# Kernel tuning notes

Hardware: AMD Instinct MI355X
Metric: run time of the kernel (lower is better)

The kernel has to match this reference:

```python
import jax, jax.numpy as jnp
import numpy as np

N_NODES = 100000
N_EDGES = 2000000
F_IN = 32
HID = 32
N_CLASS = 40


def _gru_cell(m, h, wih, whh, bih, bhh):
    # torch.nn.GRUCell math; wih/whh: [3H, H_in], gates ordered r, z, n
    gi = m @ wih.T + bih
    gh = h @ whh.T + bhh
    i_r, i_z, i_n = jnp.split(gi, 3, axis=-1)
    h_r, h_z, h_n = jnp.split(gh, 3, axis=-1)
    r = jax.nn.sigmoid(i_r + h_r)
    z = jax.nn.sigmoid(i_z + h_z)
    n = jnp.tanh(i_n + r * h_n)
    return (1.0 - z) * n + z * h


def _gated_conv(x, edge_index, edge_weight, w_proj, w_msg, wih, whh, bih, bhh):
    h = x @ w_proj                                   # [N, out]
    msg = (h @ w_msg)[edge_index[0]] * edge_weight[:, None]  # gather src -> [E, out]
    agg = jax.ops.segment_sum(msg, edge_index[1], num_segments=N_NODES)  # scatter-add to dst
    return _gru_cell(agg, h, wih, whh, bih, bhh)


def setup_inputs() -> dict:
    key = jax.random.key(0)
    ks = jax.random.split(key, 16)
    s = 0.1
    return {
        "x": jax.random.normal(ks[0], (N_NODES, F_IN), jnp.float32),
        "edge_index": jax.random.randint(ks[1], (2, N_EDGES), 0, N_NODES, jnp.int64),
        "edge_weight": jax.random.uniform(ks[2], (N_EDGES,), jnp.float32),
        "W1_proj": jax.random.normal(ks[3], (F_IN, HID), jnp.float32) * s,
        "W1_msg": jax.random.normal(ks[4], (HID, HID), jnp.float32) * s,
        "gru1_wih": jax.random.normal(ks[5], (3 * HID, HID), jnp.float32) * s,
        "gru1_whh": jax.random.normal(ks[6], (3 * HID, HID), jnp.float32) * s,
        "gru1_bih": jax.random.normal(ks[7], (3 * HID,), jnp.float32) * s,
        "gru1_bhh": jax.random.normal(ks[8], (3 * HID,), jnp.float32) * s,
        "W2_proj": jax.random.normal(ks[9], (HID, N_CLASS), jnp.float32) * s,
        "W2_msg": jax.random.normal(ks[10], (N_CLASS, N_CLASS), jnp.float32) * s,
        "gru2_wih": jax.random.normal(ks[11], (3 * N_CLASS, N_CLASS), jnp.float32) * s,
        "gru2_whh": jax.random.normal(ks[12], (3 * N_CLASS, N_CLASS), jnp.float32) * s,
        "gru2_bih": jax.random.normal(ks[13], (3 * N_CLASS,), jnp.float32) * s,
        "gru2_bhh": jax.random.normal(ks[14], (3 * N_CLASS,), jnp.float32) * s,
    }


def reference(x, edge_index, edge_weight, W1_proj, W1_msg, gru1_wih, gru1_whh,
              gru1_bih, gru1_bhh, W2_proj, W2_msg, gru2_wih, gru2_whh,
              gru2_bih, gru2_bhh):
    # eval mode: dropout is identity
    h = _gated_conv(x, edge_index, edge_weight, W1_proj, W1_msg,
                    gru1_wih, gru1_whh, gru1_bih, gru1_bhh)
    h = jax.nn.relu(h)
    h = _gated_conv(h, edge_index, edge_weight, W2_proj, W2_msg,
                    gru2_wih, gru2_whh, gru2_bih, gru2_bhh)
    return jax.nn.log_softmax(h, axis=-1)
```

## Files before the change

### kernel.cpp

```cpp
#include <hip/hip_runtime.h>
#include <math.h>

#define NN 100000
#define NP 100032
#define NE 2000000
#define FIN 32
#define H 32
#define NC 40

#define NBK 196
#define BSH 9
#define CAP 11264
#define EPT 16
#define EPB (256 * EPT)

typedef _Float16 half_t;
typedef __attribute__((ext_vector_type(8))) _Float16 half8;
typedef __attribute__((ext_vector_type(4))) _Float16 half4;
typedef __attribute__((ext_vector_type(4))) float f32x4;

__device__ __forceinline__ float sigm_(float x) {
    return 1.0f / (1.0f + __expf(-x));
}
__device__ __forceinline__ float tanh_(float x) {
    x = fminf(fmaxf(x, -20.0f), 20.0f);
    float e = __expf(2.0f * x);
    return (e - 1.0f) / (e + 1.0f);
}

__global__ __launch_bounds__(256) void kA_bucket(const int* __restrict__ ei,
                                                 const float* __restrict__ ew,
                                                 int* __restrict__ gcur,
                                                 long long* __restrict__ rec) {
    __shared__ long long recs[EPB];
    __shared__ int gdst[EPB];
    __shared__ int cnt[NBK], base[NBK], sofs[NBK];
    __shared__ int ssc[256];
    int tid = threadIdx.x;
    for (int i = tid; i < NBK; i += 256) cnt[i] = 0;
    __syncthreads();
    int e0 = blockIdx.x * EPB;
    int dcache[EPT];
#pragma unroll
    for (int i = 0; i < EPT; ++i) {
        int e = e0 + i * 256 + tid;
        dcache[i] = (e < NE) ? ei[NE + e] : -1;
        if (e < NE) atomicAdd(&cnt[dcache[i] >> BSH], 1);
    }
    __syncthreads();
    int cv = (tid < NBK) ? cnt[tid] : 0;
    ssc[tid] = cv;
    __syncthreads();
    for (int off = 1; off < 256; off <<= 1) {
        int v = (tid >= off) ? ssc[tid - off] : 0;
        __syncthreads();
        ssc[tid] += v;
        __syncthreads();
    }
    if (tid < NBK) {
        sofs[tid] = ssc[tid] - cv;
        base[tid] = atomicAdd(&gcur[tid], cv);
        cnt[tid] = 0;
    }
    __syncthreads();
#pragma unroll
    for (int i = 0; i < EPT; ++i) {
        int e = e0 + i * 256 + tid;
        if (e < NE) {
            int d = dcache[i], s = ei[e];
            int b = d >> BSH;
            int r = atomicAdd(&cnt[b], 1);
            int slot = sofs[b] + r;
            int pos = base[b] + r;
            int lo = s | ((d & 511) << 17);
            recs[slot] = (long long)(unsigned)lo |
                         ((long long)__float_as_int(ew[e]) << 32);
            gdst[slot] = (pos < CAP) ? (b * CAP + pos) : -1;
        }
    }
    __syncthreads();
    int nrec = min(EPB, NE - e0);
    for (int i = tid; i < nrec; i += 256) {
        int gd = gdst[i];
        if (gd >= 0) rec[gd] = recs[i];
    }
}

__global__ __launch_bounds__(256) void kB_sort(const int* __restrict__ gcur,
                                               const int2* __restrict__ rec,
                                               int2* __restrict__ evs,
                                               int* __restrict__ ofs,
                                               int* __restrict__ ocn) {
    __shared__ int hist[512], lofs[512], ssc[256];
    int tid = threadIdx.x, b = blockIdx.x;
    int nb0 = b << BSH;
    int nnodes = min(512, NN - nb0);
    int cntb = min(gcur[b], CAP);
    hist[tid] = 0;
    hist[tid + 256] = 0;
    __syncthreads();
    const int2* rb = rec + (size_t)b * CAP;
    for (int i = tid; i < cntb; i += 256)
        atomicAdd(&hist[(rb[i].x >> 17) & 511], 1);
    __syncthreads();
    int ps = hist[2 * tid] + hist[2 * tid + 1];
    ssc[tid] = ps;
    __syncthreads();
    for (int off = 1; off < 256; off <<= 1) {
        int v = (tid >= off) ? ssc[tid - off] : 0;
        __syncthreads();
        ssc[tid] += v;
        __syncthreads();
    }
    int ex = ssc[tid] - ps;
    lofs[2 * tid] = ex;
    lofs[2 * tid + 1] = ex + hist[2 * tid];
    __syncthreads();
    for (int l = tid; l < nnodes; l += 256) {
        ofs[nb0 + l] = b * CAP + lofs[l];
        ocn[nb0 + l] = hist[l];
    }
    hist[tid] = 0;
    hist[tid + 256] = 0;
    __syncthreads();
    int2* eb = evs + (size_t)b * CAP;
    for (int i = tid; i < cntb; i += 256) {
        int2 r = rb[i];
        int dl = (r.x >> 17) & 511;
        int rk = atomicAdd(&hist[dl], 1);
        eb[lofs[dl] + rk] = make_int2(r.x & 0x1FFFF, r.y);
    }
}

__global__ __launch_bounds__(256) void k_wpre(const float* __restrict__ W2m,
                                              const float* __restrict__ wih2,
                                              float* __restrict__ M2,
                                              int* __restrict__ gcur) {
    int i = blockIdx.x * 256 + threadIdx.x;
    if (i < NBK) gcur[i] = 0;
    if (i >= NC * 3 * NC) return;
    int u = i / (3 * NC), col = i % (3 * NC);
    float acc = 0.f;
#pragma unroll
    for (int t = 0; t < NC; ++t) acc += W2m[u * NC + t] * wih2[col * NC + t];
    M2[i] = acc;
}

__global__ __launch_bounds__(256) void k_wc(const float* __restrict__ W1m,
                                            const float* __restrict__ wih1,
                                            const float* __restrict__ W2p,
                                            const float* __restrict__ M2,
                                            const float* __restrict__ whh1,
                                            const float* __restrict__ whh2,
                                            half_t* __restrict__ W1sw,
                                            half_t* __restrict__ W2sw) {
    int i = blockIdx.x * 256 + threadIdx.x;
    if (i < 8192) {
        int j = i & 7, lane = (i >> 3) & 63, ct = (i >> 9) & 7, s = i >> 12;
        int k = s * 32 + (lane >> 4) * 8 + j;
        int col = ct * 16 + (lane & 15);
        int g = col >> 5, jj = col & 31;
        float v = 0.f;
        if (g <= 2) {
            if (k < 32) {
                float acc = 0.f;
#pragma unroll
                for (int t = 0; t < H; ++t) acc += W1m[k * H + t] * wih1[(g * H + jj) * H + t];
                v = acc;
            } else if (g < 2) {
                v = whh1[(g * H + jj) * H + (k - 32)];
            }
        } else {
            if (k >= 32) v = whh1[(2 * H + jj) * H + (k - 32)];
        }
        W1sw[i] = (half_t)v;
    } else if (i < 8192 + 18432) {
        int i2 = i - 8192;
        int j = i2 & 7, lane = (i2 >> 3) & 63;
        int tt = i2 >> 9;
        int ct = tt % 12, s = tt / 12;
        int k = s * 32 + (lane >> 4) * 8 + j;
        int col = ct * 16 + (lane & 15);
        int g = col / 48, jj = col % 48;
        float v = 0.f;
        if (jj < NC) {
            if (g <= 2) {
                if (k < 32) {
                    float acc = 0.f;
#pragma unroll
                    for (int u = 0; u < NC; ++u)
                        acc += W2p[k * NC + u] * M2[u * 3 * NC + g * NC + jj];
                    v = acc;
                } else if (k < 72 && g < 2) {
                    v = whh2[(g * NC + jj) * NC + (k - 32)];
                }
            } else {
                if (k >= 32 && k < 72) v = whh2[(2 * NC + jj) * NC + (k - 32)];
            }
        }
        W2sw[i2] = (half_t)v;
    }
}

__global__ __launch_bounds__(256) void k1_proj(const float* __restrict__ x,
                                               const float* __restrict__ Wp,
                                               half_t* __restrict__ Xc1) {
    __shared__ float sWp[FIN * H];
    __shared__ float sx[8][FIN];
    int tid = threadIdx.x;
    for (int i = tid; i < FIN * H; i += 256) sWp[i] = Wp[i];
    int nb = blockIdx.x * 8;
    int nl = tid >> 5, j = tid & 31;
    int n = nb + nl;
    if (n < NN) sx[nl][j] = x[(size_t)n * FIN + j];
    __syncthreads();
    float acc = 0.f;
#pragma unroll
    for (int k = 0; k < FIN; ++k) acc += sx[nl][k] * sWp[k * H + j];
    if (n < NN) Xc1[(size_t)n * 64 + 32 + j] = (half_t)acc;
}

__global__ __launch_bounds__(320) void k4_proj2(const half_t* __restrict__ Hh,
                                                const float* __restrict__ Wp,
                                                half_t* __restrict__ Xc2) {
    __shared__ float sWp[FIN * NC];
    __shared__ float shn[8][FIN];
    int tid = threadIdx.x;
    for (int i = tid; i < FIN * NC; i += 320) sWp[i] = Wp[i];
    int nb = blockIdx.x * 8;
    if (tid < 256) {
        int r = tid >> 5, c = tid & 31;
        shn[r][c] = (float)Hh[(size_t)(nb + r) * 32 + c];
    }
    if (tid < 192) {
        int r = tid / 24, c = tid % 24;
        Xc2[(size_t)(nb + r) * 96 + 72 + c] = (half_t)0.f;
    }
    __syncthreads();
    int nl = tid / NC, j = tid % NC;
    int n = nb + nl;
    float acc = 0.f;
#pragma unroll
    for (int k = 0; k < FIN; ++k) acc += shn[nl][k] * sWp[k * NC + j];
    if (n < NN) Xc2[(size_t)n * 96 + 32 + j] = (half_t)acc;
}

template <int SSTR4, int DSTR>
__global__ __launch_bounds__(256) void k_aggh(const int* __restrict__ ofs,
                                              const int* __restrict__ ocn,
                                              const int2* __restrict__ evs,
                                              const half_t* __restrict__ src,
                                              half_t* __restrict__ dst) {
    int idx = blockIdx.x * 256 + threadIdx.x;
    int n = idx >> 3, q = idx & 7;
    if (n >= NN) return;
    const half4* s4 = (const half4*)src + q;
    const long long* ev8 = (const long long*)evs;
    int s0 = ofs[n], c = ocn[n];
    int e1 = s0 + c;
    float acc[4] = {0.f, 0.f, 0.f, 0.f};
    int e = s0;
    for (; e + 4 <= e1; e += 4) {
        long long r0 = __builtin_nontemporal_load(ev8 + e);
        long long r1 = __builtin_nontemporal_load(ev8 + e + 1);
        long long r2 = __builtin_nontemporal_load(ev8 + e + 2);
        long long r3 = __builtin_nontemporal_load(ev8 + e + 3);
        half4 h0 = s4[(size_t)(r0 & 0x1FFFF) * SSTR4];
        half4 h1 = s4[(size_t)(r1 & 0x1FFFF) * SSTR4];
        half4 h2 = s4[(size_t)(r2 & 0x1FFFF) * SSTR4];
        half4 h3 = s4[(size_t)(r3 & 0x1FFFF) * SSTR4];
        float w0 = __int_as_float((int)(r0 >> 32));
        float w1 = __int_as_float((int)(r1 >> 32));
        float w2 = __int_as_float((int)(r2 >> 32));
        float w3 = __int_as_float((int)(r3 >> 32));
#pragma unroll
        for (int t = 0; t < 4; ++t) {
            acc[t] += w0 * (float)h0[t];
            acc[t] += w1 * (float)h1[t];
            acc[t] += w2 * (float)h2[t];
            acc[t] += w3 * (float)h3[t];
        }
    }
    for (; e < e1; ++e) {
        long long r = __builtin_nontemporal_load(ev8 + e);
        float w = __int_as_float((int)(r >> 32));
        half4 hv = s4[(size_t)(r & 0x1FFFF) * SSTR4];
#pragma unroll
        for (int t = 0; t < 4; ++t) acc[t] += w * (float)hv[t];
    }
    half4 o;
#pragma unroll
    for (int t = 0; t < 4; ++t) o[t] = (half_t)acc[t];
    *(half4*)(dst + (size_t)n * DSTR + q * 4) = o;
}

__global__ __launch_bounds__(256) void k3m(const half_t* __restrict__ Xc1,
                                           const half8* __restrict__ W1sw,
                                           const float* __restrict__ bih,
                                           const float* __restrict__ bhh,
                                           half_t* __restrict__ Hh) {
    int tid = threadIdx.x;
    int wave = tid >> 6, lane = tid & 63;
    int m16 = lane & 15, q = lane >> 4;
    int nb = blockIdx.x * 64 + wave * 16;
    const half8* xr = (const half8*)(Xc1 + (size_t)(nb + m16) * 64);
    half8 a0 = xr[q];
    half8 a1 = xr[4 + q];
    f32x4 acc[8];
#pragma unroll
    for (int ct = 0; ct < 8; ++ct) acc[ct] = (f32x4){0.f, 0.f, 0.f, 0.f};
#pragma unroll
    for (int ct = 0; ct < 8; ++ct) {
        acc[ct] = __builtin_amdgcn_mfma_f32_16x16x32_f16(a0, W1sw[ct * 64 + lane], acc[ct], 0, 0, 0);
        acc[ct] = __builtin_amdgcn_mfma_f32_16x16x32_f16(a1, W1sw[(8 + ct) * 64 + lane], acc[ct], 0, 0, 0);
    }
#pragma unroll
    for (int ct = 0; ct < 2; ++ct) {
        int j = ct * 16 + m16;
        float br = bih[j] + bhh[j];
        float bz = bih[H + j] + bhh[H + j];
        float bi = bih[2 * H + j], bh = bhh[2 * H + j];
#pragma unroll
        for (int m = 0; m < 4; ++m) {
            int node = nb + q * 4 + m;
            float r = sigm_(acc[ct][m] + br);
            float z = sigm_(acc[2 + ct][m] + bz);
            float ng = tanh_(acc[4 + ct][m] + bi + r * (acc[6 + ct][m] + bh));
            float hj = (float)Xc1[(size_t)node * 64 + 32 + j];
            float o = fmaxf((1.f - z) * ng + z * hj, 0.f);
            if (node < NN) Hh[(size_t)node * 32 + j] = (half_t)o;
        }
    }
}

__global__ __launch_bounds__(256) void k6m(const half_t* __restrict__ Xc2,
                                           const half8* __restrict__ W2sw,
                                           const float* __restrict__ bih,
                                           const float* __restrict__ bhh,
                                           float* __restrict__ out) {
    int tid = threadIdx.x;
    int wave = tid >> 6, lane = tid & 63;
    int m16 = lane & 15, q = lane >> 4;
    int nb = blockIdx.x * 64 + wave * 16;
    const half8* xr = (const half8*)(Xc2 + (size_t)(nb + m16) * 96);
    half8 a0 = xr[q], a1 = xr[4 + q], a2 = xr[8 + q];
    f32x4 acc[12];
#pragma unroll
    for (int ct = 0; ct < 12; ++ct) acc[ct] = (f32x4){0.f, 0.f, 0.f, 0.f};
#pragma unroll
    for (int ct = 0; ct < 12; ++ct) {
        acc[ct] = __builtin_amdgcn_mfma_f32_16x16x32_f16(a0, W2sw[ct * 64 + lane], acc[ct], 0, 0, 0);
        acc[ct] = __builtin_amdgcn_mfma_f32_16x16x32_f16(a1, W2sw[(12 + ct) * 64 + lane], acc[ct], 0, 0, 0);
        acc[ct] = __builtin_amdgcn_mfma_f32_16x16x32_f16(a2, W2sw[(24 + ct) * 64 + lane], acc[ct], 0, 0, 0);
    }
    float v[3][4];
#pragma unroll
    for (int ct = 0; ct < 3; ++ct) {
        int j = ct * 16 + m16;
        int jc = (j < NC) ? j : (NC - 1);
        float br = bih[jc] + bhh[jc];
        float bz = bih[NC + jc] + bhh[NC + jc];
        float bi = bih[2 * NC + jc], bh = bhh[2 * NC + jc];
#pragma unroll
        for (int m = 0; m < 4; ++m) {
            int node = nb + q * 4 + m;
            float r = sigm_(acc[ct][m] + br);
            float z = sigm_(acc[3 + ct][m] + bz);
            float ng = tanh_(acc[6 + ct][m] + bi + r * (acc[9 + ct][m] + bh));
            float hj = (float)Xc2[(size_t)node * 96 + 32 + jc];
            v[ct][m] = (1.f - z) * ng + z * hj;
        }
    }
    bool v2ok = (m16 < 8);
#pragma unroll
    for (int m = 0; m < 4; ++m) {
        float mx = fmaxf(v[0][m], v[1][m]);
        if (v2ok) mx = fmaxf(mx, v[2][m]);
#pragma unroll
        for (int d = 1; d < 16; d <<= 1) mx = fmaxf(mx, __shfl_xor(mx, d));
        float se = __expf(v[0][m] - mx) + __expf(v[1][m] - mx) +
                   (v2ok ? __expf(v[2][m] - mx) : 0.f);
#pragma unroll
        for (int d = 1; d < 16; d <<= 1) se += __shfl_xor(se, d);
        float ls = mx + __logf(se);
        int node = nb + q * 4 + m;
        if (node < NN) {
            out[(size_t)node * NC + m16] = v[0][m] - ls;
            out[(size_t)node * NC + 16 + m16] = v[1][m] - ls;
            if (v2ok) out[(size_t)node * NC + 32 + m16] = v[2][m] - ls;
        }
    }
}

extern "C" void kernel_launch(void* const* d_in, const int* in_sizes, int n_in,
                              void* d_out, int out_size, void* d_ws, size_t ws_size,
                              hipStream_t stream) {
    const float* x = (const float*)d_in[0];
    const int* ei = (const int*)d_in[1];
    const float* ew = (const float*)d_in[2];
    const float* W1p = (const float*)d_in[3];
    const float* W1m = (const float*)d_in[4];
    const float* g1wih = (const float*)d_in[5];
    const float* g1whh = (const float*)d_in[6];
    const float* g1bih = (const float*)d_in[7];
    const float* g1bhh = (const float*)d_in[8];
    const float* W2p = (const float*)d_in[9];
    const float* W2m = (const float*)d_in[10];
    const float* g2wih = (const float*)d_in[11];
    const float* g2whh = (const float*)d_in[12];
    const float* g2bih = (const float*)d_in[13];
    const float* g2bhh = (const float*)d_in[14];
    float* ws = (float*)d_ws;

    half_t* Xc = (half_t*)ws;
    half_t* Hh = (half_t*)(ws + 4801536);
    int2* rec = (int2*)ws;
    int2* evs = (int2*)(ws + 6402048);
    int* ofs = (int*)(ws + 10817536);
    int* ocn = (int*)(ws + 10917536);
    int* gcur = (int*)(ws + 11017536);
    half_t* W1sw = (half_t*)(ws + 11017792);
    half_t* W2sw = W1sw + 8192;
    float* M2 = ws + 11031104;
    float* out = (float*)d_out;

    k_wpre<<<(NC * 3 * NC + 255) / 256, 256, 0, stream>>>(W2m, g2wih, M2, gcur);
    kA_bucket<<<(NE + EPB - 1) / EPB, 256, 0, stream>>>(ei, ew, gcur, (long long*)rec);
    kB_sort<<<NBK, 256, 0, stream>>>(gcur, rec, evs, ofs, ocn);
    k_wc<<<(8192 + 18432 + 255) / 256, 256, 0, stream>>>(
        W1m, g1wih, W2p, M2, g1whh, g2whh, W1sw, W2sw);

    k1_proj<<<NN / 8, 256, 0, stream>>>(x, W1p, Xc);
    k_aggh<16, 64><<<(NN * 8 + 255) / 256, 256, 0, stream>>>(ofs, ocn, evs, Xc + 32, Xc);
    k3m<<<NP / 64, 256, 0, stream>>>(Xc, (const half8*)W1sw, g1bih, g1bhh, Hh);

    k4_proj2<<<NN / 8, 320, 0, stream>>>(Hh, W2p, Xc);
    k_aggh<8, 96><<<(NN * 8 + 255) / 256, 256, 0, stream>>>(ofs, ocn, evs, Hh, Xc);
    k6m<<<NP / 64, 256, 0, stream>>>(Xc, (const half8*)W2sw, g2bih, g2bhh, out);
}
```

Before: 313.2 us.

## Split per-node edge lists into source-range slices with block-synchronized gather

The bucket sort now bins edges by destination and by one of four source-index ranges. Each node's offsets and counts are stored per slice, with the four counts packed as 8-bit fields. The aggregation kernel walks the slices in order and calls __syncthreads between them, so all threads of a block gather from the same region of the source feature array together, aiming for better L2 locality. Layer 1 also writes a compact 32-wide copy of the projected features so the gather reads rows half as wide. The costs are more offset arrays, extra block barriers, and a silent limit of 255 edges per node per slice; bucket capacity is also lowered.

```diff
diff --git a/kernel.cpp b/kernel.cpp
--- a/kernel.cpp
+++ b/kernel.cpp
@@ -10,7 +10,8 @@
 
 #define NBK 196
 #define BSH 9
-#define CAP 11264
+#define CAP 10880
+#define NSL 4
 #define EPT 16
 #define EPB (256 * EPT)
 
@@ -89,22 +90,29 @@
 __global__ __launch_bounds__(256) void kB_sort(const int* __restrict__ gcur,
                                                const int2* __restrict__ rec,
                                                int2* __restrict__ evs,
-                                               int* __restrict__ ofs,
-                                               int* __restrict__ ocn) {
-    __shared__ int hist[512], lofs[512], ssc[256];
+                                               int* __restrict__ ofs2,
+                                               int* __restrict__ cnt4) {
+    __shared__ int hist[2048], lofs[2048], ssc[256];
     int tid = threadIdx.x, b = blockIdx.x;
     int nb0 = b << BSH;
     int nnodes = min(512, NN - nb0);
     int cntb = min(gcur[b], CAP);
-    hist[tid] = 0;
-    hist[tid + 256] = 0;
+    for (int i = tid; i < 2048; i += 256) hist[i] = 0;
     __syncthreads();
     const int2* rb = rec + (size_t)b * CAP;
-    for (int i = tid; i < cntb; i += 256)
-        atomicAdd(&hist[(rb[i].x >> 17) & 511], 1);
-    __syncthreads();
-    int ps = hist[2 * tid] + hist[2 * tid + 1];
-    ssc[tid] = ps;
+    for (int i = tid; i < cntb; i += 256) {
+        int rx = rb[i].x;
+        int bin = (((rx & 0x1FFFF) >> 15) << BSH) | ((rx >> 17) & 511);
+        atomicAdd(&hist[bin], 1);
+    }
+    __syncthreads();
+    int base = tid * 8, ls = 0, lh[8];
+#pragma unroll
+    for (int j = 0; j < 8; ++j) {
+        lh[j] = hist[base + j];
+        ls += lh[j];
+    }
+    ssc[tid] = ls;
     __syncthreads();
     for (int off = 1; off < 256; off <<= 1) {
         int v = (tid >= off) ? ssc[tid - off] : 0;
@@ -112,23 +120,30 @@
         ssc[tid] += v;
         __syncthreads();
     }
-    int ex = ssc[tid] - ps;
-    lofs[2 * tid] = ex;
-    lofs[2 * tid + 1] = ex + hist[2 * tid];
+    int ex = ssc[tid] - ls;
+#pragma unroll
+    for (int j = 0; j < 8; ++j) {
+        lofs[base + j] = ex;
+        ex += lh[j];
+    }
     __syncthreads();
     for (int l = tid; l < nnodes; l += 256) {
-        ofs[nb0 + l] = b * CAP + lofs[l];
-        ocn[nb0 + l] = hist[l];
-    }
-    hist[tid] = 0;
-    hist[tid + 256] = 0;
+        int c0 = hist[l], c1 = hist[512 + l], c2 = hist[1024 + l], c3 = hist[1536 + l];
+        cnt4[nb0 + l] = c0 | (c1 << 8) | (c2 << 16) | (c3 << 24);
+        ofs2[0 * NN + nb0 + l] = b * CAP + lofs[l];
+        ofs2[1 * NN + nb0 + l] = b * CAP + lofs[512 + l];
+        ofs2[2 * NN + nb0 + l] = b * CAP + lofs[1024 + l];
+        ofs2[3 * NN + nb0 + l] = b * CAP + lofs[1536 + l];
+    }
+    __syncthreads();
+    for (int i = tid; i < 2048; i += 256) hist[i] = 0;
     __syncthreads();
     int2* eb = evs + (size_t)b * CAP;
     for (int i = tid; i < cntb; i += 256) {
         int2 r = rb[i];
-        int dl = (r.x >> 17) & 511;
-        int rk = atomicAdd(&hist[dl], 1);
-        eb[lofs[dl] + rk] = make_int2(r.x & 0x1FFFF, r.y);
+        int bin = (((r.x & 0x1FFFF) >> 15) << BSH) | ((r.x >> 17) & 511);
+        int rk = atomicAdd(&hist[bin], 1);
+        eb[lofs[bin] + rk] = make_int2(r.x & 0x1FFFF, r.y);
     }
 }
 
@@ -204,7 +219,8 @@
 
 __global__ __launch_bounds__(256) void k1_proj(const float* __restrict__ x,
                                                const float* __restrict__ Wp,
-                                               half_t* __restrict__ Xc1) {
+                                               half_t* __restrict__ Xc1,
+                                               half_t* __restrict__ Hd) {
     __shared__ float sWp[FIN * H];
     __shared__ float sx[8][FIN];
     int tid = threadIdx.x;
@@ -217,7 +233,11 @@
     float acc = 0.f;
 #pragma unroll
     for (int k = 0; k < FIN; ++k) acc += sx[nl][k] * sWp[k * H + j];
-    if (n < NN) Xc1[(size_t)n * 64 + 32 + j] = (half_t)acc;
+    if (n < NN) {
+        half_t hv = (half_t)acc;
+        Xc1[(size_t)n * 64 + 32 + j] = hv;
+        Hd[(size_t)n * 32 + j] = hv;
+    }
 }
 
 __global__ __launch_bounds__(320) void k4_proj2(const half_t* __restrict__ Hh,
@@ -245,48 +265,51 @@
     if (n < NN) Xc2[(size_t)n * 96 + 32 + j] = (half_t)acc;
 }
 
-template <int SSTR4, int DSTR>
-__global__ __launch_bounds__(256) void k_aggh(const int* __restrict__ ofs,
-                                              const int* __restrict__ ocn,
+template <int DSTR>
+__global__ __launch_bounds__(256) void k_aggh(const int* __restrict__ ofs2,
+                                              const int* __restrict__ cnt4,
                                               const int2* __restrict__ evs,
                                               const half_t* __restrict__ src,
                                               half_t* __restrict__ dst) {
     int idx = blockIdx.x * 256 + threadIdx.x;
     int n = idx >> 3, q = idx & 7;
-    if (n >= NN) return;
     const half4* s4 = (const half4*)src + q;
     const long long* ev8 = (const long long*)evs;
-    int s0 = ofs[n], c = ocn[n];
-    int e1 = s0 + c;
+    int cw = cnt4[n];
     float acc[4] = {0.f, 0.f, 0.f, 0.f};
-    int e = s0;
-    for (; e + 4 <= e1; e += 4) {
-        long long r0 = __builtin_nontemporal_load(ev8 + e);
-        long long r1 = __builtin_nontemporal_load(ev8 + e + 1);
-        long long r2 = __builtin_nontemporal_load(ev8 + e + 2);
-        long long r3 = __builtin_nontemporal_load(ev8 + e + 3);
-        half4 h0 = s4[(size_t)(r0 & 0x1FFFF) * SSTR4];
-        half4 h1 = s4[(size_t)(r1 & 0x1FFFF) * SSTR4];
-        half4 h2 = s4[(size_t)(r2 & 0x1FFFF) * SSTR4];
-        half4 h3 = s4[(size_t)(r3 & 0x1FFFF) * SSTR4];
-        float w0 = __int_as_float((int)(r0 >> 32));
-        float w1 = __int_as_float((int)(r1 >> 32));
-        float w2 = __int_as_float((int)(r2 >> 32));
-        float w3 = __int_as_float((int)(r3 >> 32));
-#pragma unroll
-        for (int t = 0; t < 4; ++t) {
-            acc[t] += w0 * (float)h0[t];
-            acc[t] += w1 * (float)h1[t];
-            acc[t] += w2 * (float)h2[t];
-            acc[t] += w3 * (float)h3[t];
-        }
-    }
-    for (; e < e1; ++e) {
-        long long r = __builtin_nontemporal_load(ev8 + e);
-        float w = __int_as_float((int)(r >> 32));
-        half4 hv = s4[(size_t)(r & 0x1FFFF) * SSTR4];
-#pragma unroll
-        for (int t = 0; t < 4; ++t) acc[t] += w * (float)hv[t];
+    for (int s = 0; s < NSL; ++s) {
+        int s0 = ofs2[s * NN + n];
+        int e1 = s0 + ((cw >> (8 * s)) & 255);
+        int e = s0;
+        for (; e + 4 <= e1; e += 4) {
+            long long r0 = __builtin_nontemporal_load(ev8 + e);
+            long long r1 = __builtin_nontemporal_load(ev8 + e + 1);
+            long long r2 = __builtin_nontemporal_load(ev8 + e + 2);
+            long long r3 = __builtin_nontemporal_load(ev8 + e + 3);
+            half4 h0 = s4[(size_t)(r0 & 0x1FFFF) * 8];
+            half4 h1 = s4[(size_t)(r1 & 0x1FFFF) * 8];
+            half4 h2 = s4[(size_t)(r2 & 0x1FFFF) * 8];
+            half4 h3 = s4[(size_t)(r3 & 0x1FFFF) * 8];
+            float w0 = __int_as_float((int)(r0 >> 32));
+            float w1 = __int_as_float((int)(r1 >> 32));
+            float w2 = __int_as_float((int)(r2 >> 32));
+            float w3 = __int_as_float((int)(r3 >> 32));
+#pragma unroll
+            for (int t = 0; t < 4; ++t) {
+                acc[t] += w0 * (float)h0[t];
+                acc[t] += w1 * (float)h1[t];
+                acc[t] += w2 * (float)h2[t];
+                acc[t] += w3 * (float)h3[t];
+            }
+        }
+        for (; e < e1; ++e) {
+            long long r = __builtin_nontemporal_load(ev8 + e);
+            float w = __int_as_float((int)(r >> 32));
+            half4 hv = s4[(size_t)(r & 0x1FFFF) * 8];
+#pragma unroll
+            for (int t = 0; t < 4; ++t) acc[t] += w * (float)hv[t];
+        }
+        __syncthreads();
     }
     half4 o;
 #pragma unroll
@@ -413,28 +436,29 @@
     float* ws = (float*)d_ws;
 
     half_t* Xc = (half_t*)ws;
+    half_t* Hd = (half_t*)(ws + 3201024);
     half_t* Hh = (half_t*)(ws + 4801536);
     int2* rec = (int2*)ws;
     int2* evs = (int2*)(ws + 6402048);
-    int* ofs = (int*)(ws + 10817536);
-    int* ocn = (int*)(ws + 10917536);
-    int* gcur = (int*)(ws + 11017536);
-    half_t* W1sw = (half_t*)(ws + 11017792);
+    int* ofs2 = (int*)(ws + 10667008);
+    int* cnt4 = (int*)(ws + 11067008);
+    int* gcur = (int*)(ws + 11167008);
+    half_t* W1sw = (half_t*)(ws + 11167264);
     half_t* W2sw = W1sw + 8192;
-    float* M2 = ws + 11031104;
+    float* M2 = ws + 11180576;
     float* out = (float*)d_out;
 
     k_wpre<<<(NC * 3 * NC + 255) / 256, 256, 0, stream>>>(W2m, g2wih, M2, gcur);
     kA_bucket<<<(NE + EPB - 1) / EPB, 256, 0, stream>>>(ei, ew, gcur, (long long*)rec);
-    kB_sort<<<NBK, 256, 0, stream>>>(gcur, rec, evs, ofs, ocn);
+    kB_sort<<<NBK, 256, 0, stream>>>(gcur, rec, evs, ofs2, cnt4);
     k_wc<<<(8192 + 18432 + 255) / 256, 256, 0, stream>>>(
         W1m, g1wih, W2p, M2, g1whh, g2whh, W1sw, W2sw);
 
-    k1_proj<<<NN / 8, 256, 0, stream>>>(x, W1p, Xc);
-    k_aggh<16, 64><<<(NN * 8 + 255) / 256, 256, 0, stream>>>(ofs, ocn, evs, Xc + 32, Xc);
+    k1_proj<<<NN / 8, 256, 0, stream>>>(x, W1p, Xc, Hd);
+    k_aggh<64><<<NN * 8 / 256, 256, 0, stream>>>(ofs2, cnt4, evs, Hd, Xc);
     k3m<<<NP / 64, 256, 0, stream>>>(Xc, (const half8*)W1sw, g1bih, g1bhh, Hh);
 
     k4_proj2<<<NN / 8, 320, 0, stream>>>(Hh, W2p, Xc);
-    k_aggh<8, 96><<<(NN * 8 + 255) / 256, 256, 0, stream>>>(ofs, ocn, evs, Hh, Xc);
+    k_aggh<96><<<NN * 8 / 256, 256, 0, stream>>>(ofs2, cnt4, evs, Hh, Xc);
     k6m<<<NP / 64, 256, 0, stream>>>(Xc, (const half8*)W2sw, g2bih, g2bhh, out);
 }
```

Result: slower. 326.2 us (+4.2%).
